# Optimization experiments

Measured on AMD Instinct MI355X. Metric: run time of the kernel, lower is better.

The kernel has to match this reference:

```python
import jax, jax.numpy as jnp
import numpy as np

DIM = 1024
NUM_HEADS = 16
REL_DIM = 32
B, N = 8, 512


def setup_inputs() -> dict:
    key = jax.random.key(0)
    ks = jax.random.split(key, 8)
    s = 0.02
    return {
        "x": jax.random.normal(ks[0], (B, N, DIM), dtype=jnp.float32),
        "rel_bias": jax.random.normal(ks[1], (B, N, N, REL_DIM), dtype=jnp.float32),
        # torch nn.Linear convention: weight (out_features, in_features)
        "W_qkv": jax.random.normal(ks[2], (3 * DIM, DIM), dtype=jnp.float32) * s,
        "b_qkv": jax.random.normal(ks[3], (3 * DIM,), dtype=jnp.float32) * s,
        "W_rel": jax.random.normal(ks[4], (NUM_HEADS, REL_DIM), dtype=jnp.float32) * s,
        "b_rel": jax.random.normal(ks[5], (NUM_HEADS,), dtype=jnp.float32) * s,
        "W_out": jax.random.normal(ks[6], (DIM, DIM), dtype=jnp.float32) * s,
        "b_out": jax.random.normal(ks[7], (DIM,), dtype=jnp.float32) * s,
    }


def reference(x, rel_bias, W_qkv, b_qkv, W_rel, b_rel, W_out, b_out):
    Bx, Nx, D = x.shape
    H = NUM_HEADS
    hd = D // H
    # QKV projection: (B,N,3D) -> (B,N,3,H,hd)
    qkv = (x @ W_qkv.T + b_qkv).reshape(Bx, Nx, 3, H, hd)
    q, k, v = qkv[:, :, 0], qkv[:, :, 1], qkv[:, :, 2]
    scale = hd ** -0.5
    attn = jnp.einsum('bnhd,bmhd->bhnm', q, k) * scale
    # per-pair relative bias projected to heads: (B,N,N,H) -> (B,H,N,N)
    rel = (rel_bias @ W_rel.T + b_rel).transpose(0, 3, 1, 2)
    attn = jax.nn.softmax(attn + rel, axis=-1)
    out = jnp.einsum('bhnm,bmhd->bnhd', attn, v).reshape(Bx, Nx, D)
    return out @ W_out.T + b_out
```

## Files before the change

### kernel.cpp

```cpp
#include <hip/hip_runtime.h>

typedef unsigned short u16;
typedef unsigned int u32;
typedef __attribute__((ext_vector_type(8))) __bf16 bf16x8;
typedef __attribute__((ext_vector_type(4))) float f32x4;

union U8 {
  bf16x8 b;
  uint2 u2[2];
  uint4 u4;
  u16 us[8];
};

__device__ __forceinline__ u16 f2bf(float f) {
  u32 x = __float_as_uint(f);
  x += 0x7FFFu + ((x >> 16) & 1u);
  return (u16)(x >> 16);
}
__device__ __forceinline__ float bf2f(u16 u) {
  return __uint_as_float(((u32)u) << 16);
}

#define GLOAD16(gp, lp)                                                          \
  __builtin_amdgcn_global_load_lds(                                              \
      (const __attribute__((address_space(1))) unsigned int*)(const void*)(gp),  \
      (__attribute__((address_space(3))) unsigned int*)(void*)(lp), 16, 0, 0)

__global__ void k_convert_all(const float* __restrict__ x, const float* __restrict__ wq,
                              const float* __restrict__ wo, u16* __restrict__ xb,
                              u16* __restrict__ wqb, u16* __restrict__ wob) {
  const int NX = 1048576, NQ = 786432, NO = 262144;
  int idx = blockIdx.x * blockDim.x + threadIdx.x;
  int stride = gridDim.x * blockDim.x;
  for (int i = idx; i < NX + NQ + NO; i += stride) {
    const float4* s;
    ushort4* d;
    int k;
    if (i < NX) { s = (const float4*)x; d = (ushort4*)xb; k = i; }
    else if (i < NX + NQ) { s = (const float4*)wq; d = (ushort4*)wqb; k = i - NX; }
    else { s = (const float4*)wo; d = (ushort4*)wob; k = i - NX - NQ; }
    float4 v = s[k];
    ushort4 o;
    o.x = f2bf(v.x); o.y = f2bf(v.y); o.z = f2bf(v.z); o.w = f2bf(v.w);
    d[k] = o;
  }
}

__global__ __launch_bounds__(256) void k_rel(const float* __restrict__ rb,
                                             const float* __restrict__ Wr,
                                             const float* __restrict__ br,
                                             u16* __restrict__ out) {
  const int t = threadIdx.x;
  const int i16 = t & 15, j = (t >> 4) & 3, c = t >> 6;
  const int mt = blockIdx.x, ntg = blockIdx.y, b = blockIdx.z;
  const int nt = ntg >> 2, g = ntg & 3;
  const int n = nt * 16 + 4 * g + j;
  const int m = mt * 64 + c * 16 + i16;

  const float4* rp = (const float4*)(rb + ((size_t)(b * 512 + n) * 512 + m) * 32);
  float4 r4[8];
#pragma unroll
  for (int q = 0; q < 8; ++q) r4[q] = rp[q];

  const size_t obase =
      (((size_t)(b * 16) * 32 + nt) * 8 + mt) * 1024 + c * 256 + (g * 16 + i16) * 4 + j;
#pragma unroll
  for (int h = 0; h < 16; ++h) {
    float acc = br[h];
    const float* w = Wr + h * 32;
#pragma unroll
    for (int q = 0; q < 8; ++q) {
      acc += r4[q].x * w[4 * q + 0] + r4[q].y * w[4 * q + 1] +
             r4[q].z * w[4 * q + 2] + r4[q].w * w[4 * q + 3];
    }
    out[obase + (size_t)h * 262144] = f2bf(acc);
  }
}

template <int MODE>
__global__ __launch_bounds__(256) void k_gemm(const u16* __restrict__ A,
                                              const u16* __restrict__ Bm,
                                              const float* __restrict__ bias,
                                              u16* __restrict__ Qo, u16* __restrict__ Ko,
                                              u16* __restrict__ Vo, float* __restrict__ Co,
                                              int K) {
  __shared__ u16 Al[128 * 64];
  __shared__ u16 Bl[128 * 64];
  const int t = threadIdx.x;
  const int lane = t & 63, wid = t >> 6;
  const int g = lane >> 4, i16 = lane & 15;
  const int wm = wid >> 1, wn = wid & 1;
  const int bm = blockIdx.y, bn = blockIdx.x;

  f32x4 zero = {0.f, 0.f, 0.f, 0.f};
  f32x4 acc[4][4];
#pragma unroll
  for (int mi = 0; mi < 4; ++mi)
#pragma unroll
    for (int ni = 0; ni < 4; ++ni) acc[mi][ni] = zero;

  int srow[4], sgc[4];
#pragma unroll
  for (int i = 0; i < 4; ++i) {
    int ch = wid * 256 + i * 64 + lane;
    int r = ch >> 3, cs = ch & 7;
    srow[i] = r;
    sgc[i] = cs ^ (r & 7);
  }

  for (int k0 = 0; k0 < K; k0 += 64) {
    __syncthreads();
#pragma unroll
    for (int i = 0; i < 4; ++i) {
      const u16* ga = A + (size_t)(bm * 128 + srow[i]) * K + k0 + sgc[i] * 8;
      const u16* gb = Bm + (size_t)(bn * 128 + srow[i]) * K + k0 + sgc[i] * 8;
      GLOAD16(ga, Al + (size_t)(wid * 256 + i * 64) * 8);
      GLOAD16(gb, Bl + (size_t)(wid * 256 + i * 64) * 8);
    }
    __syncthreads();

#pragma unroll
    for (int kk = 0; kk < 2; ++kk) {
      U8 af[4], bfr[4];
#pragma unroll
      for (int mi = 0; mi < 4; ++mi) {
        int row = wm * 64 + mi * 16 + i16;
        int ch = (g + 4 * kk) ^ (row & 7);
        af[mi].u4 = *(const uint4*)(Al + row * 64 + ch * 8);
      }
#pragma unroll
      for (int ni = 0; ni < 4; ++ni) {
        int row = wn * 64 + ni * 16 + i16;
        int ch = (g + 4 * kk) ^ (row & 7);
        bfr[ni].u4 = *(const uint4*)(Bl + row * 64 + ch * 8);
      }
#pragma unroll
      for (int mi = 0; mi < 4; ++mi)
#pragma unroll
        for (int ni = 0; ni < 4; ++ni)
          acc[mi][ni] = __builtin_amdgcn_mfma_f32_16x16x32_bf16(af[mi].b, bfr[ni].b,
                                                                acc[mi][ni], 0, 0, 0);
    }
  }

#pragma unroll
  for (int mi = 0; mi < 4; ++mi) {
#pragma unroll
    for (int ni = 0; ni < 4; ++ni) {
      int col = bn * 128 + wn * 64 + ni * 16 + i16;
      int row0 = bm * 128 + wm * 64 + mi * 16 + 4 * g;
      float bia = bias[col];
      if (MODE == 0) {
        int tt = col >> 10;
        int h = (col >> 6) & 15;
        int d = col & 63;
        int b = row0 >> 9;
        int n0 = row0 & 511;
        if (tt < 2) {
          u16* dst = (tt == 0) ? Qo : Ko;
#pragma unroll
          for (int j = 0; j < 4; ++j)
            dst[((size_t)(b * 16 + h) * 512 + n0 + j) * 64 + d] = f2bf(acc[mi][ni][j] + bia);
        } else {
          uint2 w;
          w.x = (u32)f2bf(acc[mi][ni][0] + bia) | ((u32)f2bf(acc[mi][ni][1] + bia) << 16);
          w.y = (u32)f2bf(acc[mi][ni][2] + bia) | ((u32)f2bf(acc[mi][ni][3] + bia) << 16);
          *(uint2*)(Vo + ((size_t)(b * 16 + h) * 64 + d) * 512 + n0) = w;
        }
      } else {
#pragma unroll
        for (int j = 0; j < 4; ++j)
          Co[(size_t)(row0 + j) * 1024 + col] = acc[mi][ni][j] + bia;
      }
    }
  }
}

__global__ __launch_bounds__(256) void k_attn(const u16* __restrict__ Q,
                                              const u16* __restrict__ Kb,
                                              const u16* __restrict__ Vtb,
                                              const u16* __restrict__ Rel,
                                              u16* __restrict__ Out) {
  __shared__ u16 Kl[2][64 * 64];
  __shared__ u16 Vl[2][64 * 64];
  __shared__ u16 Pl[4][16 * 68];

  const int qt = blockIdx.x, h = blockIdx.y, b = blockIdx.z;
  const int t = threadIdx.x, lane = t & 63, wid = t >> 6;
  const int g = lane >> 4, i16 = lane & 15;
  const size_t bh = (size_t)(b * 16 + h);

  const u16* Qg = Q + (bh * 512 + qt * 64 + wid * 16 + i16) * 64;
  U8 qf[2];
  qf[0].u4 = *(const uint4*)(Qg + 8 * g);
  qf[1].u4 = *(const uint4*)(Qg + 8 * g + 32);

  float m_run[4], l_run[4];
  f32x4 zero = {0.f, 0.f, 0.f, 0.f};
  f32x4 acc[4];
#pragma unroll
  for (int c = 0; c < 4; ++c) acc[c] = zero;
#pragma unroll
  for (int j = 0; j < 4; ++j) { m_run[j] = -1e30f; l_run[j] = 0.f; }

  int srow[2], sgc[2];
#pragma unroll
  for (int i = 0; i < 2; ++i) {
    int ch = wid * 128 + i * 64 + lane;
    int r = ch >> 3, cs = ch & 7;
    srow[i] = r;
    sgc[i] = cs ^ (r & 7);
  }

  const u16* Kg0 = Kb + bh * 512 * 64;
  const u16* Vg0 = Vtb + bh * 64 * 512;
  const u16* Rg = Rel + ((bh * 32 + qt * 4 + wid) * 8) * 1024 + lane * 4;

#define STAGE(buf, m0)                                                                  \
  do {                                                                                  \
    _Pragma("unroll") for (int i = 0; i < 2; ++i) {                                     \
      GLOAD16(Kg0 + (size_t)((m0) + srow[i]) * 64 + sgc[i] * 8,                         \
              &Kl[buf][(size_t)(wid * 128 + i * 64) * 8]);                              \
      GLOAD16(Vg0 + (size_t)srow[i] * 512 + (m0) + sgc[i] * 8,                          \
              &Vl[buf][(size_t)(wid * 128 + i * 64) * 8]);                              \
    }                                                                                   \
  } while (0)

  STAGE(0, 0);
  __syncthreads();

  for (int it = 0; it < 8; ++it) {
    const int buf = it & 1;
    if (it < 7) STAGE(buf ^ 1, it * 64 + 64);

    uint2 rl[4];
#pragma unroll
    for (int c = 0; c < 4; ++c) rl[c] = *(const uint2*)(Rg + it * 1024 + c * 256);

    f32x4 s[4];
#pragma unroll
    for (int c = 0; c < 4; ++c) s[c] = zero;
    __builtin_amdgcn_s_setprio(1);
#pragma unroll
    for (int c = 0; c < 4; ++c) {
#pragma unroll
      for (int kk = 0; kk < 2; ++kk) {
        int row = c * 16 + i16;
        int ch = (g + 4 * kk) ^ (row & 7);
        U8 kf;
        kf.u4 = *(const uint4*)(&Kl[buf][row * 64 + ch * 8]);
        s[c] = __builtin_amdgcn_mfma_f32_16x16x32_bf16(qf[kk].b, kf.b, s[c], 0, 0, 0);
      }
    }
    __builtin_amdgcn_s_setprio(0);

#pragma unroll
    for (int c = 0; c < 4; ++c) {
      const u16* rc = (const u16*)&rl[c];
#pragma unroll
      for (int j = 0; j < 4; ++j) s[c][j] = s[c][j] * 0.125f + bf2f(rc[j]);
    }
    float fac[4];
#pragma unroll
    for (int j = 0; j < 4; ++j) {
      float pm = fmaxf(fmaxf(s[0][j], s[1][j]), fmaxf(s[2][j], s[3][j]));
      pm = fmaxf(pm, __shfl_xor(pm, 1));
      pm = fmaxf(pm, __shfl_xor(pm, 2));
      pm = fmaxf(pm, __shfl_xor(pm, 4));
      pm = fmaxf(pm, __shfl_xor(pm, 8));
      float mnew = fmaxf(m_run[j], pm);
      fac[j] = __expf(m_run[j] - mnew);
      m_run[j] = mnew;
    }
#pragma unroll
    for (int c = 0; c < 4; ++c)
#pragma unroll
      for (int j = 0; j < 4; ++j) s[c][j] = __expf(s[c][j] - m_run[j]);
#pragma unroll
    for (int j = 0; j < 4; ++j) {
      float rs = s[0][j] + s[1][j] + s[2][j] + s[3][j];
      rs += __shfl_xor(rs, 1);
      rs += __shfl_xor(rs, 2);
      rs += __shfl_xor(rs, 4);
      rs += __shfl_xor(rs, 8);
      l_run[j] = l_run[j] * fac[j] + rs;
    }
#pragma unroll
    for (int c = 0; c < 4; ++c)
#pragma unroll
      for (int j = 0; j < 4; ++j) acc[c][j] *= fac[j];

    u16* Pw = Pl[wid];
#pragma unroll
    for (int c = 0; c < 4; ++c)
#pragma unroll
      for (int j = 0; j < 4; ++j)
        Pw[(4 * g + j) * 68 + c * 16 + i16] = f2bf(s[c][j]);
    __syncthreads();

    U8 pf[2];
#pragma unroll
    for (int kk = 0; kk < 2; ++kk) {
      const u16* p = Pl[wid] + i16 * 68 + 8 * g + 32 * kk;
      pf[kk].u2[0] = *(const uint2*)p;
      pf[kk].u2[1] = *(const uint2*)(p + 4);
    }
    __builtin_amdgcn_s_setprio(1);
#pragma unroll
    for (int c = 0; c < 4; ++c) {
#pragma unroll
      for (int kk = 0; kk < 2; ++kk) {
        int row = c * 16 + i16;
        int ch = (g + 4 * kk) ^ (row & 7);
        U8 vf;
        vf.u4 = *(const uint4*)(&Vl[buf][row * 64 + ch * 8]);
        acc[c] = __builtin_amdgcn_mfma_f32_16x16x32_bf16(pf[kk].b, vf.b, acc[c], 0, 0, 0);
      }
    }
    __builtin_amdgcn_s_setprio(0);
    __syncthreads();
  }
#undef STAGE

#pragma unroll
  for (int c = 0; c < 4; ++c) {
#pragma unroll
    for (int j = 0; j < 4; ++j) {
      int n = qt * 64 + wid * 16 + 4 * g + j;
      float v = acc[c][j] / l_run[j];
      Out[((size_t)b * 512 + n) * 1024 + h * 64 + c * 16 + i16] = f2bf(v);
    }
  }
}

extern "C" void kernel_launch(void* const* d_in, const int* in_sizes, int n_in,
                              void* d_out, int out_size, void* d_ws, size_t ws_size,
                              hipStream_t stream) {
  const float* x = (const float*)d_in[0];
  const float* rel_bias = (const float*)d_in[1];
  const float* W_qkv = (const float*)d_in[2];
  const float* b_qkv = (const float*)d_in[3];
  const float* W_rel = (const float*)d_in[4];
  const float* b_rel = (const float*)d_in[5];
  const float* W_out = (const float*)d_in[6];
  const float* b_out = (const float*)d_in[7];
  float* out = (float*)d_out;

  char* ws = (char*)d_ws;
  u16* x_bf    = (u16*)(ws);
  u16* wqkv_bf = (u16*)(ws + 8388608);
  u16* wout_bf = (u16*)(ws + 14680064);
  u16* Qw      = (u16*)(ws + 16777216);
  u16* Kw      = (u16*)(ws + 25165824);
  u16* Vt      = (u16*)(ws + 33554432);
  u16* relb    = (u16*)(ws + 41943040);
  u16* attno   = (u16*)(ws + 109051904);

  k_convert_all<<<2048, 256, 0, stream>>>(x, W_qkv, W_out, x_bf, wqkv_bf, wout_bf);

  k_rel<<<dim3(8, 128, 8), 256, 0, stream>>>(rel_bias, W_rel, b_rel, relb);

  k_gemm<0><<<dim3(24, 32), 256, 0, stream>>>(x_bf, wqkv_bf, b_qkv, Qw, Kw, Vt, nullptr, 1024);

  k_attn<<<dim3(8, 16, 8), 256, 0, stream>>>(Qw, Kw, Vt, relb, attno);

  k_gemm<1><<<dim3(8, 32), 256, 0, stream>>>(attno, wout_bf, b_out, nullptr, nullptr, nullptr,
                                             out, 1024);
}
```

Baseline: 186.8 us.

## Compute rel-bias projection with MFMA and split out-projection GEMM into smaller tiles

The relative-bias projection kernel now converts rel_bias rows to bf16 and uses a 16x16x32 MFMA against the bf16 W_rel with the bias preloaded into the accumulator. Each thread covers 16 query rows instead of one, so the grid is four times smaller and the output is written as packed 16-byte stores. The output-projection GEMM becomes its own kernel with 128x64 tiles, doubling its block count to 512 so more CUs are busy. Packed bf16 conversion via v_cvt_pk_bf16_f32 replaces manual rounding in several places. Rounding rel_bias and W_rel to bf16 before the product adds some precision loss.

Result: slower. 200.0 us (+7.1%).

```diff
diff --git a/kernel.cpp b/kernel.cpp
--- a/kernel.cpp
+++ b/kernel.cpp
@@ -9,6 +9,7 @@
   bf16x8 b;
   uint2 u2[2];
   uint4 u4;
+  u32 w[4];
   u16 us[8];
 };
 
@@ -19,6 +20,11 @@
 }
 __device__ __forceinline__ float bf2f(u16 u) {
   return __uint_as_float(((u32)u) << 16);
+}
+__device__ __forceinline__ u32 cvtpk(float lo, float hi) {
+  u32 r;
+  asm("v_cvt_pk_bf16_f32 %0, %1, %2" : "=v"(r) : "v"(lo), "v"(hi));
+  return r;
 }
 
 #define GLOAD16(gp, lp)                                                          \
@@ -51,39 +57,62 @@
                                              const float* __restrict__ br,
                                              u16* __restrict__ out) {
   const int t = threadIdx.x;
-  const int i16 = t & 15, j = (t >> 4) & 3, c = t >> 6;
-  const int mt = blockIdx.x, ntg = blockIdx.y, b = blockIdx.z;
-  const int nt = ntg >> 2, g = ntg & 3;
-  const int n = nt * 16 + 4 * g + j;
-  const int m = mt * 64 + c * 16 + i16;
-
-  const float4* rp = (const float4*)(rb + ((size_t)(b * 512 + n) * 512 + m) * 32);
-  float4 r4[8];
-#pragma unroll
-  for (int q = 0; q < 8; ++q) r4[q] = rp[q];
-
-  const size_t obase =
-      (((size_t)(b * 16) * 32 + nt) * 8 + mt) * 1024 + c * 256 + (g * 16 + i16) * 4 + j;
-#pragma unroll
-  for (int h = 0; h < 16; ++h) {
-    float acc = br[h];
-    const float* w = Wr + h * 32;
-#pragma unroll
-    for (int q = 0; q < 8; ++q) {
-      acc += r4[q].x * w[4 * q + 0] + r4[q].y * w[4 * q + 1] +
-             r4[q].z * w[4 * q + 2] + r4[q].w * w[4 * q + 3];
-    }
-    out[obase + (size_t)h * 262144] = f2bf(acc);
-  }
-}
-
-template <int MODE>
-__global__ __launch_bounds__(256) void k_gemm(const u16* __restrict__ A,
-                                              const u16* __restrict__ Bm,
-                                              const float* __restrict__ bias,
-                                              u16* __restrict__ Qo, u16* __restrict__ Ko,
-                                              u16* __restrict__ Vo, float* __restrict__ Co,
-                                              int K) {
+  const int lane = t & 63, c2 = t >> 6;
+  const int i16 = lane & 15, g4 = lane >> 4;
+  const int mt = blockIdx.x, nt = blockIdx.y, b = blockIdx.z;
+
+  U8 wb;
+  {
+    const float* wp = Wr + i16 * 32 + 8 * g4;
+    float4 w0 = *(const float4*)wp;
+    float4 w1 = *(const float4*)(wp + 4);
+    wb.w[0] = cvtpk(w0.x, w0.y);
+    wb.w[1] = cvtpk(w0.z, w0.w);
+    wb.w[2] = cvtpk(w1.x, w1.y);
+    wb.w[3] = cvtpk(w1.z, w1.w);
+  }
+  const float bias = br[i16];
+
+  const int m = mt * 64 + c2 * 16 + i16;
+  const float* rbase = rb + ((size_t)(b * 512 + nt * 16) * 512 + m) * 32 + 8 * g4;
+
+  f32x4 accv[16];
+#pragma unroll
+  for (int ni = 0; ni < 16; ++ni) {
+    float4 a0 = *(const float4*)(rbase + (size_t)ni * 16384);
+    float4 a1 = *(const float4*)(rbase + (size_t)ni * 16384 + 4);
+    U8 af;
+    af.w[0] = cvtpk(a0.x, a0.y);
+    af.w[1] = cvtpk(a0.z, a0.w);
+    af.w[2] = cvtpk(a1.x, a1.y);
+    af.w[3] = cvtpk(a1.z, a1.w);
+    f32x4 ci = {bias, bias, bias, bias};
+    accv[ni] = __builtin_amdgcn_mfma_f32_16x16x32_bf16(af.b, wb.b, ci, 0, 0, 0);
+  }
+
+  const size_t base =
+      ((((size_t)(b * 16 + i16)) * 32 + nt) * 8 + mt) * 1024 + c2 * 256 + g4 * 16;
+#pragma unroll
+  for (int gp = 0; gp < 4; ++gp) {
+    u32 wd[8];
+#pragma unroll
+    for (int w = 0; w < 8; ++w) {
+      int jj = w >> 1, jlo = 2 * (w & 1);
+      wd[w] = cvtpk(accv[4 * gp + jlo][jj], accv[4 * gp + jlo + 1][jj]);
+    }
+    uint4 s0 = {wd[0], wd[1], wd[2], wd[3]};
+    uint4 s1 = {wd[4], wd[5], wd[6], wd[7]};
+    *(uint4*)(out + base + gp * 64) = s0;
+    *(uint4*)(out + base + gp * 64 + 8) = s1;
+  }
+}
+
+__global__ __launch_bounds__(256) void k_gemm_qkv(const u16* __restrict__ A,
+                                                  const u16* __restrict__ Bm,
+                                                  const float* __restrict__ bias,
+                                                  u16* __restrict__ Qo, u16* __restrict__ Ko,
+                                                  u16* __restrict__ Vo) {
+  const int K = 1024;
   __shared__ u16 Al[128 * 64];
   __shared__ u16 Bl[128 * 64];
   const int t = threadIdx.x;
@@ -150,28 +179,107 @@
       int col = bn * 128 + wn * 64 + ni * 16 + i16;
       int row0 = bm * 128 + wm * 64 + mi * 16 + 4 * g;
       float bia = bias[col];
-      if (MODE == 0) {
-        int tt = col >> 10;
-        int h = (col >> 6) & 15;
-        int d = col & 63;
-        int b = row0 >> 9;
-        int n0 = row0 & 511;
-        if (tt < 2) {
-          u16* dst = (tt == 0) ? Qo : Ko;
-#pragma unroll
-          for (int j = 0; j < 4; ++j)
-            dst[((size_t)(b * 16 + h) * 512 + n0 + j) * 64 + d] = f2bf(acc[mi][ni][j] + bia);
-        } else {
-          uint2 w;
-          w.x = (u32)f2bf(acc[mi][ni][0] + bia) | ((u32)f2bf(acc[mi][ni][1] + bia) << 16);
-          w.y = (u32)f2bf(acc[mi][ni][2] + bia) | ((u32)f2bf(acc[mi][ni][3] + bia) << 16);
-          *(uint2*)(Vo + ((size_t)(b * 16 + h) * 64 + d) * 512 + n0) = w;
-        }
+      int tt = col >> 10;
+      int h = (col >> 6) & 15;
+      int d = col & 63;
+      int b = row0 >> 9;
+      int n0 = row0 & 511;
+      if (tt < 2) {
+        u16* dst = (tt == 0) ? Qo : Ko;
+#pragma unroll
+        for (int j = 0; j < 4; ++j)
+          dst[((size_t)(b * 16 + h) * 512 + n0 + j) * 64 + d] = f2bf(acc[mi][ni][j] + bia);
       } else {
-#pragma unroll
-        for (int j = 0; j < 4; ++j)
-          Co[(size_t)(row0 + j) * 1024 + col] = acc[mi][ni][j] + bia;
-      }
+        uint2 w;
+        w.x = cvtpk(acc[mi][ni][0] + bia, acc[mi][ni][1] + bia);
+        w.y = cvtpk(acc[mi][ni][2] + bia, acc[mi][ni][3] + bia);
+        *(uint2*)(Vo + ((size_t)(b * 16 + h) * 64 + d) * 512 + n0) = w;
+      }
+    }
+  }
+}
+
+__global__ __launch_bounds__(256) void k_gemm_out(const u16* __restrict__ A,
+                                                  const u16* __restrict__ Bm,
+                                                  const float* __restrict__ bias,
+                                                  float* __restrict__ Co) {
+  const int K = 1024;
+  __shared__ u16 Al[128 * 64];
+  __shared__ u16 Bl[64 * 64];
+  const int t = threadIdx.x;
+  const int lane = t & 63, wid = t >> 6;
+  const int g = lane >> 4, i16 = lane & 15;
+  const int bm = blockIdx.y, bn = blockIdx.x;
+
+  f32x4 zero = {0.f, 0.f, 0.f, 0.f};
+  f32x4 acc[2][4];
+#pragma unroll
+  for (int mi = 0; mi < 2; ++mi)
+#pragma unroll
+    for (int ni = 0; ni < 4; ++ni) acc[mi][ni] = zero;
+
+  int srowA[4], sgcA[4], srowB[2], sgcB[2];
+#pragma unroll
+  for (int i = 0; i < 4; ++i) {
+    int ch = wid * 256 + i * 64 + lane;
+    int r = ch >> 3, cs = ch & 7;
+    srowA[i] = r;
+    sgcA[i] = cs ^ (r & 7);
+  }
+#pragma unroll
+  for (int i = 0; i < 2; ++i) {
+    int ch = wid * 128 + i * 64 + lane;
+    int r = ch >> 3, cs = ch & 7;
+    srowB[i] = r;
+    sgcB[i] = cs ^ (r & 7);
+  }
+
+  for (int k0 = 0; k0 < K; k0 += 64) {
+    __syncthreads();
+#pragma unroll
+    for (int i = 0; i < 4; ++i)
+      GLOAD16(A + (size_t)(bm * 128 + srowA[i]) * K + k0 + sgcA[i] * 8,
+              Al + (size_t)(wid * 256 + i * 64) * 8);
+#pragma unroll
+    for (int i = 0; i < 2; ++i)
+      GLOAD16(Bm + (size_t)(bn * 64 + srowB[i]) * K + k0 + sgcB[i] * 8,
+              Bl + (size_t)(wid * 128 + i * 64) * 8);
+    __syncthreads();
+
+#pragma unroll
+    for (int kk = 0; kk < 2; ++kk) {
+      U8 af[2], bfr[4];
+#pragma unroll
+      for (int mi = 0; mi < 2; ++mi) {
+        int row = wid * 32 + mi * 16 + i16;
+        int ch = (g + 4 * kk) ^ (row & 7);
+        af[mi].u4 = *(const uint4*)(Al + row * 64 + ch * 8);
+      }
+#pragma unroll
+      for (int ni = 0; ni < 4; ++ni) {
+        int row = ni * 16 + i16;
+        int ch = (g + 4 * kk) ^ (row & 7);
+        bfr[ni].u4 = *(const uint4*)(Bl + row * 64 + ch * 8);
+      }
+#pragma unroll
+      for (int mi = 0; mi < 2; ++mi)
+#pragma unroll
+        for (int ni = 0; ni < 4; ++ni)
+          acc[mi][ni] = __builtin_amdgcn_mfma_f32_16x16x32_bf16(af[mi].b, bfr[ni].b,
+                                                                acc[mi][ni], 0, 0, 0);
+    }
+  }
+
+#pragma unroll
+  for (int mi = 0; mi < 2; ++mi) {
+#pragma unroll
+    for (int ni = 0; ni < 4; ++ni) {
+      int col = bn * 64 + ni * 16 + i16;
+      int row0 = bm * 128 + wid * 32 + mi * 16 + 4 * g;
+      float bia = bias[col];
+#pragma unroll
+      for (int j = 0; j < 4; ++j)
+        Co[(size_t)(row0 + j) * 1024 + col] = acc[mi][ni][j] + bia;
     }
   }
 }
@@ -358,12 +466,11 @@
 
   k_convert_all<<<2048, 256, 0, stream>>>(x, W_qkv, W_out, x_bf, wqkv_bf, wout_bf);
 
-  k_rel<<<dim3(8, 128, 8), 256, 0, stream>>>(rel_bias, W_rel, b_rel, relb);
-
-  k_gemm<0><<<dim3(24, 32), 256, 0, stream>>>(x_bf, wqkv_bf, b_qkv, Qw, Kw, Vt, nullptr, 1024);
+  k_rel<<<dim3(8, 32, 8), 256, 0, stream>>>(rel_bias, W_rel, b_rel, relb);
+
+  k_gemm_qkv<<<dim3(24, 32), 256, 0, stream>>>(x_bf, wqkv_bf, b_qkv, Qw, Kw, Vt);
 
   k_attn<<<dim3(8, 16, 8), 256, 0, stream>>>(Qw, Kw, Vt, relb, attno);
 
-  k_gemm<1><<<dim3(8, 32), 256, 0, stream>>>(attno, wout_bf, b_out, nullptr, nullptr, nullptr,
-                                             out, 1024);
-}
+  k_gemm_out<<<dim3(16, 32), 256, 0, stream>>>(attno, wout_bf, b_out, out);
+}
```
